# Kernel tuning notes

Measured on AMD Instinct MI355X. Metric: run time of the kernel, lower is better.

The kernel has to match this reference:

```python
import jax, jax.numpy as jnp
import numpy as np

B, N1, N2, C1, C2, MLP_OUT = 16, 4096, 1024, 128, 256, 256


def setup_inputs() -> dict:
    key = jax.random.key(0)
    k = jax.random.split(key, 8)
    xyz1 = jax.random.normal(k[0], (B, N1, 3), dtype=jnp.float32)
    feat1 = jax.random.normal(k[1], (B, N1, C1), dtype=jnp.float32)
    xyz2 = jax.random.normal(k[2], (B, N2, 3), dtype=jnp.float32)
    feat2 = jax.random.normal(k[3], (B, N2, C2), dtype=jnp.float32)
    d_in = C1 + C2
    W1 = jax.random.normal(k[4], (d_in, MLP_OUT), dtype=jnp.float32) / np.sqrt(d_in)
    b1 = jnp.zeros((MLP_OUT,), dtype=jnp.float32)
    W2 = jax.random.normal(k[5], (MLP_OUT, MLP_OUT), dtype=jnp.float32) / np.sqrt(MLP_OUT)
    b2 = jnp.zeros((MLP_OUT,), dtype=jnp.float32)
    return {"xyz1": xyz1, "feat1": feat1, "xyz2": xyz2, "feat2": feat2,
            "W1": W1, "b1": b1, "W2": W2, "b2": b2}


def reference(xyz1, feat1, xyz2, feat2, W1, b1, W2, b2):
    # squared pairwise distances [B, N1, N2]
    dists = jnp.sum((xyz1[:, :, None, :] - xyz2[:, None, :, :]) ** 2, axis=-1)
    # 3 nearest neighbors (smallest distances)
    neg_d3, idx = jax.lax.top_k(-dists, 3)      # [B, N1, 3]
    d3 = jnp.maximum(-neg_d3, 1e-10)
    w = 1.0 / d3
    w = w / jnp.sum(w, axis=-1, keepdims=True)   # [B, N1, 3]
    # gather neighbor features: [B, N1, 3, C2]
    neighbor_feats = jax.vmap(lambda f, i: f[i])(feat2, idx)
    interpolated = jnp.sum(w[..., None] * neighbor_feats, axis=2)  # [B, N1, C2]
    new_feat = jnp.concatenate([interpolated, feat1], axis=-1)     # [B, N1, C2+C1]
    h = jax.nn.relu(new_feat @ W1 + b1)
    return jax.nn.relu(h @ W2 + b2)
```

## Files before the change

### kernel.cpp

```cpp
#include <hip/hip_runtime.h>
#include <cstdint>
#include <cstddef>

typedef unsigned short ushort_t;
typedef unsigned int uint_t;

typedef __bf16 bf16x8 __attribute__((ext_vector_type(8)));
typedef float floatx4 __attribute__((ext_vector_type(4)));

#define B_ 16
#define N1_ 4096
#define N2_ 1024
#define C1_ 128
#define C2_ 256
#define DIN_ 384
#define DOUT_ 256
#define M_ (B_ * N1_)

#define ASTRIDE 392
#define HSTRIDE 264


__device__ __forceinline__ ushort_t f2bf(float f) {
  unsigned int u = __builtin_bit_cast(unsigned int, f);
  u = (u + 0x7fffu + ((u >> 16) & 1u)) >> 16;
  return (ushort_t)u;
}


__global__ __launch_bounds__(256) void prep_kernel(
    const float* __restrict__ W1, const float* __restrict__ W2,
    ushort_t* __restrict__ W1s, ushort_t* __restrict__ W2s) {
  int e = blockIdx.x * 256 + threadIdx.x;
  if (e < DOUT_ * DIN_) {
    int kk = e & 31, n = (e >> 5) & 255, t = e >> 13;
    W1s[e] = f2bf(W1[(size_t)(t * 32 + kk) * DOUT_ + n]);
  }
  if (e < DOUT_ * DOUT_) {
    int kk = e & 31, n = (e >> 5) & 255, t = e >> 13;
    W2s[e] = f2bf(W2[(size_t)(t * 32 + kk) * DOUT_ + n]);
  }
}


__device__ __forceinline__ void ins_exact(float& s0, float& s1, float& s2,
                                          int& i0, int& i1, int& i2,
                                          float d, int p) {
  float ns2 = __builtin_amdgcn_fmed3f(d, s1, s2);
  float ns1 = __builtin_amdgcn_fmed3f(d, s0, s1);
  float ns0 = fminf(d, s0);
  bool c0 = d < s0, c1 = d < s1, c2 = d < s2;
  i2 = c1 ? i1 : (c2 ? p : i2);
  i1 = c0 ? i0 : (c1 ? p : i1);
  i0 = c0 ? p : i0;
  s0 = ns0; s1 = ns1; s2 = ns2;
}

__device__ __forceinline__ void ins_merge(float& s0, float& s1, float& s2,
                                          int& i0, int& i1, int& i2,
                                          float e, int j) {
  bool t0 = (e < s0) || (e == s0 && j < i0);
  bool t1 = (e < s1) || (e == s1 && j < i1);
  bool t2 = (e < s2) || (e == s2 && j < i2);
  s2 = t1 ? s1 : (t2 ? e : s2);
  i2 = t1 ? i1 : (t2 ? j : i2);
  s1 = t0 ? s0 : (t1 ? e : s1);
  i1 = t0 ? i0 : (t1 ? j : i1);
  s0 = t0 ? e : s0;
  i0 = t0 ? j : i0;
}

__global__ __launch_bounds__(256) void knn_kernel(
    const float* __restrict__ xyz1, const float* __restrict__ xyz2,
    int* __restrict__ idx_out, float* __restrict__ w_out) {
  __shared__ float4 xs4[N2_];
  int b = blockIdx.x >> 7;
  int n1base = (blockIdx.x & 127) << 5;
  const float* p2 = xyz2 + (size_t)b * N2_ * 3;
  for (int i = threadIdx.x; i < N2_; i += 256) {
    const float* s = p2 + 3 * i;
    xs4[i] = make_float4(s[0], s[1], s[2], 0.0f);
  }
  __syncthreads();

  int g = threadIdx.x >> 3;
  int sub = threadIdx.x & 7;
  int row = b * N1_ + n1base + g;
  const float* p1 = xyz1 + (size_t)row * 3;
  float x1 = p1[0], y1 = p1[1], z1 = p1[2];

  float s0 = 3.0e38f, s1 = 3.0e38f, s2 = 3.0e38f;
  int i0 = 0, i1 = 0, i2 = 0;

  int p = sub;
#pragma unroll 8
  for (int t = 0; t < N2_ / 8; ++t) {
    float4 qv = xs4[p];
    float dx = x1 - qv.x;
    float dy = y1 - qv.y;
    float dz = z1 - qv.z;
    float d = dx * dx + dy * dy + dz * dz;
    ins_exact(s0, s1, s2, i0, i1, i2, d, p);
    p += 8;
  }

#pragma unroll
  for (int mm = 1; mm <= 4; mm <<= 1) {
    float e0 = __shfl_xor(s0, mm), e1 = __shfl_xor(s1, mm), e2 = __shfl_xor(s2, mm);
    int j0 = __shfl_xor(i0, mm), j1 = __shfl_xor(i1, mm), j2 = __shfl_xor(i2, mm);
    ins_merge(s0, s1, s2, i0, i1, i2, e0, j0);
    ins_merge(s0, s1, s2, i0, i1, i2, e1, j1);
    ins_merge(s0, s1, s2, i0, i1, i2, e2, j2);
  }

  if (sub == 0) {
    float r0 = 1.0f / fmaxf(s0, 1e-10f);
    float r1 = 1.0f / fmaxf(s1, 1e-10f);
    float r2 = 1.0f / fmaxf(s2, 1e-10f);
    float s = 1.0f / (r0 + r1 + r2);
    int base = row * 3;
    idx_out[base + 0] = i0;
    idx_out[base + 1] = i1;
    idx_out[base + 2] = i2;
    w_out[base + 0] = r0 * s;
    w_out[base + 1] = r1 * s;
    w_out[base + 2] = r2 * s;
  }
}


__global__ __launch_bounds__(256, 3) void fused_kernel(
    const float* __restrict__ feat1, const float* __restrict__ feat2,
    const int* __restrict__ idx, const float* __restrict__ w,
    const ushort_t* __restrict__ W1s, const float* __restrict__ b1,
    const ushort_t* __restrict__ W2s, const float* __restrict__ b2,
    float* __restrict__ out) {
  __shared__ ushort_t As[64 * ASTRIDE];
  const int tid = threadIdx.x;
  const int wave = tid >> 6;
  const int lane = tid & 63;
  const int m = lane & 15;
  const int q = lane >> 4;
  const int row0 = blockIdx.x * 64;
  const int b = row0 >> 12;

  const int b_off = (wave * 64 + m) * 32 + q * 8;

  bf16x8 bf0[4], bf1[4];
#pragma unroll
  for (int j = 0; j < 4; ++j) bf0[j] = *(const bf16x8*)(W1s + b_off + j * 512);

#pragma unroll 8
  for (int it = 0; it < 16; ++it) {
    int rl = wave * 16 + it;
    int row = row0 + rl;
    const int* ip = idx + (size_t)row * 3;
    const float* wp = w + (size_t)row * 3;
    int i0 = ip[0], i1 = ip[1], i2 = ip[2];
    float w0 = wp[0], w1 = wp[1], w2 = wp[2];

    const float4* f0 = (const float4*)(feat2 + ((size_t)b * N2_ + i0) * C2_);
    const float4* f1 = (const float4*)(feat2 + ((size_t)b * N2_ + i1) * C2_);
    const float4* f2 = (const float4*)(feat2 + ((size_t)b * N2_ + i2) * C2_);
    float4 a = f0[lane];
    float4 c = f1[lane];
    float4 d = f2[lane];
    float vx = w0 * a.x + w1 * c.x + w2 * d.x;
    float vy = w0 * a.y + w1 * c.y + w2 * d.y;
    float vz = w0 * a.z + w1 * c.z + w2 * d.z;
    float vw = w0 * a.w + w1 * c.w + w2 * d.w;
    uint_t lo = (uint_t)f2bf(vx) | ((uint_t)f2bf(vy) << 16);
    uint_t hi = (uint_t)f2bf(vz) | ((uint_t)f2bf(vw) << 16);
    *(uint2*)&As[rl * ASTRIDE + 4 * lane] = make_uint2(lo, hi);

    float2 t1 = ((const float2*)(feat1 + (size_t)row * C1_))[lane];
    uint_t pk = (uint_t)f2bf(t1.x) | ((uint_t)f2bf(t1.y) << 16);
    *(uint_t*)&As[rl * ASTRIDE + 256 + 2 * lane] = pk;
  }
  __syncthreads();

  floatx4 acc[4][4];
#pragma unroll
  for (int i = 0; i < 4; ++i)
#pragma unroll
    for (int j = 0; j < 4; ++j) acc[i][j] = (floatx4)0.0f;

  {
    bf16x8 af[4];
#pragma unroll
    for (int t = 0; t < 12; t += 2) {
#pragma unroll
      for (int j = 0; j < 4; ++j)
        bf1[j] = *(const bf16x8*)(W1s + (size_t)(t + 1) * 8192 + b_off + j * 512);
#pragma unroll
      for (int i = 0; i < 4; ++i)
        af[i] = *(const bf16x8*)&As[(m + 16 * i) * ASTRIDE + t * 32 + q * 8];
#pragma unroll
      for (int i = 0; i < 4; ++i)
#pragma unroll
        for (int j = 0; j < 4; ++j)
          acc[i][j] = __builtin_amdgcn_mfma_f32_16x16x32_bf16(af[i], bf0[j],
                                                              acc[i][j], 0, 0, 0);
      if (t + 2 < 12) {
#pragma unroll
        for (int j = 0; j < 4; ++j)
          bf0[j] = *(const bf16x8*)(W1s + (size_t)(t + 2) * 8192 + b_off + j * 512);
      }
#pragma unroll
      for (int i = 0; i < 4; ++i)
        af[i] = *(const bf16x8*)&As[(m + 16 * i) * ASTRIDE + (t + 1) * 32 + q * 8];
#pragma unroll
      for (int i = 0; i < 4; ++i)
#pragma unroll
        for (int j = 0; j < 4; ++j)
          acc[i][j] = __builtin_amdgcn_mfma_f32_16x16x32_bf16(af[i], bf1[j],
                                                              acc[i][j], 0, 0, 0);
    }
  }

#pragma unroll
  for (int j = 0; j < 4; ++j) bf0[j] = *(const bf16x8*)(W2s + b_off + j * 512);

  __syncthreads();

  ushort_t* HS = As;
#pragma unroll
  for (int j = 0; j < 4; ++j) {
    int col = wave * 64 + j * 16 + m;
    float bv = b1[col];
#pragma unroll
    for (int i = 0; i < 4; ++i)
#pragma unroll
      for (int r = 0; r < 4; ++r) {
        int row = i * 16 + q * 4 + r;
        float v = acc[i][j][r] + bv;
        v = v > 0.0f ? v : 0.0f;
        HS[row * HSTRIDE + col] = f2bf(v);
      }
  }
  __syncthreads();

  floatx4 acc2[4][4];
#pragma unroll
  for (int i = 0; i < 4; ++i)
#pragma unroll
    for (int j = 0; j < 4; ++j) acc2[i][j] = (floatx4)0.0f;

  {
    bf16x8 af[4];
#pragma unroll
    for (int t = 0; t < 8; t += 2) {
#pragma unroll
      for (int j = 0; j < 4; ++j)
        bf1[j] = *(const bf16x8*)(W2s + (size_t)(t + 1) * 8192 + b_off + j * 512);
#pragma unroll
      for (int i = 0; i < 4; ++i)
        af[i] = *(const bf16x8*)&HS[(m + 16 * i) * HSTRIDE + t * 32 + q * 8];
#pragma unroll
      for (int i = 0; i < 4; ++i)
#pragma unroll
        for (int j = 0; j < 4; ++j)
          acc2[i][j] = __builtin_amdgcn_mfma_f32_16x16x32_bf16(af[i], bf0[j],
                                                               acc2[i][j], 0, 0, 0);
      if (t + 2 < 8) {
#pragma unroll
        for (int j = 0; j < 4; ++j)
          bf0[j] = *(const bf16x8*)(W2s + (size_t)(t + 2) * 8192 + b_off + j * 512);
      }
#pragma unroll
      for (int i = 0; i < 4; ++i)
        af[i] = *(const bf16x8*)&HS[(m + 16 * i) * HSTRIDE + (t + 1) * 32 + q * 8];
#pragma unroll
      for (int i = 0; i < 4; ++i)
#pragma unroll
        for (int j = 0; j < 4; ++j)
          acc2[i][j] = __builtin_amdgcn_mfma_f32_16x16x32_bf16(af[i], bf1[j],
                                                               acc2[i][j], 0, 0, 0);
    }
  }

#pragma unroll
  for (int j = 0; j < 4; ++j) {
    int col = wave * 64 + j * 16 + m;
    float bv = b2[col];
#pragma unroll
    for (int i = 0; i < 4; ++i)
#pragma unroll
      for (int r = 0; r < 4; ++r) {
        int row = i * 16 + q * 4 + r;
        float v = acc2[i][j][r] + bv;
        v = v > 0.0f ? v : 0.0f;
        out[(size_t)(row0 + row) * DOUT_ + col] = v;
      }
  }
}


constexpr size_t OFF_W1S = 0;
constexpr size_t OFF_W2S = OFF_W1S + 196608;
constexpr size_t OFF_IDX = OFF_W2S + 131072;
constexpr size_t OFF_W = OFF_IDX + 786432;
constexpr size_t WS_TOTAL = OFF_W + 786432;

extern "C" void kernel_launch(void* const* d_in, const int* in_sizes, int n_in,
                              void* d_out, int out_size, void* d_ws, size_t ws_size,
                              hipStream_t stream) {
  const float* xyz1 = (const float*)d_in[0];
  const float* feat1 = (const float*)d_in[1];
  const float* xyz2 = (const float*)d_in[2];
  const float* feat2 = (const float*)d_in[3];
  const float* W1 = (const float*)d_in[4];
  const float* b1 = (const float*)d_in[5];
  const float* W2 = (const float*)d_in[6];
  const float* b2 = (const float*)d_in[7];

  if (ws_size < WS_TOTAL) return;

  char* ws = (char*)d_ws;
  ushort_t* W1s = (ushort_t*)(ws + OFF_W1S);
  ushort_t* W2s = (ushort_t*)(ws + OFF_W2S);
  int* idx = (int*)(ws + OFF_IDX);
  float* w = (float*)(ws + OFF_W);

  prep_kernel<<<384, 256, 0, stream>>>(W1, W2, W1s, W2s);
  knn_kernel<<<B_ * (N1_ / 32), 256, 0, stream>>>(xyz1, xyz2, idx, w);
  fused_kernel<<<M_ / 64, 256, 0, stream>>>(feat1, feat2, idx, w, W1s, b1, W2s,
                                            b2, (float*)d_out);
}
```

Measured before the change: 196.4 us.

## Use one thread per query in KNN and 8-wave 2x4 tiling in fused MLP

The KNN kernel drops the 8-lane split per query and its shuffle merge. Each thread now scans all 1024 reference points itself, in 128-thread blocks, and writes the result directly. The fused MLP kernel goes from 4 to 8 waves per 64-row block, with each wave computing a 32x64 output tile instead of 64x64. Register double-buffering of weight fragments is removed so that more waves can be resident. This trades explicit load pipelining and LDS fragment reuse for higher occupancy, and the KNN change cuts the grid to 512 blocks, which may leave the GPU underfilled.

New measurement: 233.4 us. +18.8%, slower.

```diff
diff --git a/kernel.cpp b/kernel.cpp
--- a/kernel.cpp
+++ b/kernel.cpp
@@ -43,93 +43,61 @@
 }
 
 
-__device__ __forceinline__ void ins_exact(float& s0, float& s1, float& s2,
-                                          int& i0, int& i1, int& i2,
-                                          float d, int p) {
-  float ns2 = __builtin_amdgcn_fmed3f(d, s1, s2);
-  float ns1 = __builtin_amdgcn_fmed3f(d, s0, s1);
-  float ns0 = fminf(d, s0);
-  bool c0 = d < s0, c1 = d < s1, c2 = d < s2;
-  i2 = c1 ? i1 : (c2 ? p : i2);
-  i1 = c0 ? i0 : (c1 ? p : i1);
-  i0 = c0 ? p : i0;
-  s0 = ns0; s1 = ns1; s2 = ns2;
-}
-
-__device__ __forceinline__ void ins_merge(float& s0, float& s1, float& s2,
-                                          int& i0, int& i1, int& i2,
-                                          float e, int j) {
-  bool t0 = (e < s0) || (e == s0 && j < i0);
-  bool t1 = (e < s1) || (e == s1 && j < i1);
-  bool t2 = (e < s2) || (e == s2 && j < i2);
-  s2 = t1 ? s1 : (t2 ? e : s2);
-  i2 = t1 ? i1 : (t2 ? j : i2);
-  s1 = t0 ? s0 : (t1 ? e : s1);
-  i1 = t0 ? i0 : (t1 ? j : i1);
-  s0 = t0 ? e : s0;
-  i0 = t0 ? j : i0;
-}
-
-__global__ __launch_bounds__(256) void knn_kernel(
+__global__ __launch_bounds__(128) void knn_kernel(
     const float* __restrict__ xyz1, const float* __restrict__ xyz2,
     int* __restrict__ idx_out, float* __restrict__ w_out) {
   __shared__ float4 xs4[N2_];
-  int b = blockIdx.x >> 7;
-  int n1base = (blockIdx.x & 127) << 5;
+  const int b = blockIdx.x >> 5;
+  const int chunk = blockIdx.x & 31;
   const float* p2 = xyz2 + (size_t)b * N2_ * 3;
-  for (int i = threadIdx.x; i < N2_; i += 256) {
+  for (int i = threadIdx.x; i < N2_; i += 128) {
     const float* s = p2 + 3 * i;
     xs4[i] = make_float4(s[0], s[1], s[2], 0.0f);
   }
   __syncthreads();
 
-  int g = threadIdx.x >> 3;
-  int sub = threadIdx.x & 7;
-  int row = b * N1_ + n1base + g;
+  const int row = b * N1_ + chunk * 128 + threadIdx.x;
   const float* p1 = xyz1 + (size_t)row * 3;
-  float x1 = p1[0], y1 = p1[1], z1 = p1[2];
+  const float x1 = p1[0], y1 = p1[1], z1 = p1[2];
 
   float s0 = 3.0e38f, s1 = 3.0e38f, s2 = 3.0e38f;
   int i0 = 0, i1 = 0, i2 = 0;
 
-  int p = sub;
-#pragma unroll 8
-  for (int t = 0; t < N2_ / 8; ++t) {
-    float4 qv = xs4[p];
-    float dx = x1 - qv.x;
-    float dy = y1 - qv.y;
-    float dz = z1 - qv.z;
-    float d = dx * dx + dy * dy + dz * dz;
-    ins_exact(s0, s1, s2, i0, i1, i2, d, p);
-    p += 8;
-  }
-
-#pragma unroll
-  for (int mm = 1; mm <= 4; mm <<= 1) {
-    float e0 = __shfl_xor(s0, mm), e1 = __shfl_xor(s1, mm), e2 = __shfl_xor(s2, mm);
-    int j0 = __shfl_xor(i0, mm), j1 = __shfl_xor(i1, mm), j2 = __shfl_xor(i2, mm);
-    ins_merge(s0, s1, s2, i0, i1, i2, e0, j0);
-    ins_merge(s0, s1, s2, i0, i1, i2, e1, j1);
-    ins_merge(s0, s1, s2, i0, i1, i2, e2, j2);
-  }
-
-  if (sub == 0) {
-    float r0 = 1.0f / fmaxf(s0, 1e-10f);
-    float r1 = 1.0f / fmaxf(s1, 1e-10f);
-    float r2 = 1.0f / fmaxf(s2, 1e-10f);
-    float s = 1.0f / (r0 + r1 + r2);
-    int base = row * 3;
-    idx_out[base + 0] = i0;
-    idx_out[base + 1] = i1;
-    idx_out[base + 2] = i2;
-    w_out[base + 0] = r0 * s;
-    w_out[base + 1] = r1 * s;
-    w_out[base + 2] = r2 * s;
-  }
-}
-
-
-__global__ __launch_bounds__(256, 3) void fused_kernel(
+  for (int o = 0; o < N2_; o += 16) {
+#pragma unroll
+    for (int i = 0; i < 16; ++i) {
+      float4 qv = xs4[o + i];
+      float dx = x1 - qv.x;
+      float dy = y1 - qv.y;
+      float dz = z1 - qv.z;
+      float d = dx * dx + dy * dy + dz * dz;
+      bool c0 = d < s0, c1 = d < s1, c2 = d < s2;
+      float ns2 = __builtin_amdgcn_fmed3f(d, s1, s2);
+      float ns1 = __builtin_amdgcn_fmed3f(d, s0, s1);
+      float ns0 = fminf(d, s0);
+      int p = o + i;
+      i2 = c1 ? i1 : (c2 ? p : i2);
+      i1 = c0 ? i0 : (c1 ? p : i1);
+      i0 = c0 ? p : i0;
+      s0 = ns0; s1 = ns1; s2 = ns2;
+    }
+  }
+
+  float r0 = 1.0f / fmaxf(s0, 1e-10f);
+  float r1 = 1.0f / fmaxf(s1, 1e-10f);
+  float r2 = 1.0f / fmaxf(s2, 1e-10f);
+  float s = 1.0f / (r0 + r1 + r2);
+  int base = row * 3;
+  idx_out[base + 0] = i0;
+  idx_out[base + 1] = i1;
+  idx_out[base + 2] = i2;
+  w_out[base + 0] = r0 * s;
+  w_out[base + 1] = r1 * s;
+  w_out[base + 2] = r2 * s;
+}
+
+
+__global__ __launch_bounds__(512, 6) void fused_kernel(
     const float* __restrict__ feat1, const float* __restrict__ feat2,
     const int* __restrict__ idx, const float* __restrict__ w,
     const ushort_t* __restrict__ W1s, const float* __restrict__ b1,
@@ -141,18 +109,16 @@
   const int lane = tid & 63;
   const int m = lane & 15;
   const int q = lane >> 4;
+  const int wm = wave & 1;
+  const int wn = wave >> 1;
   const int row0 = blockIdx.x * 64;
   const int b = row0 >> 12;
 
-  const int b_off = (wave * 64 + m) * 32 + q * 8;
-
-  bf16x8 bf0[4], bf1[4];
-#pragma unroll
-  for (int j = 0; j < 4; ++j) bf0[j] = *(const bf16x8*)(W1s + b_off + j * 512);
-
-#pragma unroll 8
-  for (int it = 0; it < 16; ++it) {
-    int rl = wave * 16 + it;
+  const int b_off = (wn * 64 + m) * 32 + q * 8;
+
+#pragma unroll
+  for (int it = 0; it < 8; ++it) {
+    int rl = wave * 8 + it;
     int row = row0 + rl;
     const int* ip = idx + (size_t)row * 3;
     const float* wp = w + (size_t)row * 3;
@@ -179,60 +145,40 @@
   }
   __syncthreads();
 
-  floatx4 acc[4][4];
-#pragma unroll
-  for (int i = 0; i < 4; ++i)
+  floatx4 acc[2][4];
+#pragma unroll
+  for (int i = 0; i < 2; ++i)
 #pragma unroll
     for (int j = 0; j < 4; ++j) acc[i][j] = (floatx4)0.0f;
 
-  {
-    bf16x8 af[4];
-#pragma unroll
-    for (int t = 0; t < 12; t += 2) {
+#pragma unroll 2
+  for (int t = 0; t < 12; ++t) {
+    bf16x8 bfr[4], af[2];
+#pragma unroll
+    for (int j = 0; j < 4; ++j)
+      bfr[j] = *(const bf16x8*)(W1s + (size_t)t * 8192 + b_off + j * 512);
+#pragma unroll
+    for (int i = 0; i < 2; ++i)
+      af[i] = *(const bf16x8*)&As[(wm * 32 + m + 16 * i) * ASTRIDE + t * 32 + q * 8];
+#pragma unroll
+    for (int i = 0; i < 2; ++i)
 #pragma unroll
       for (int j = 0; j < 4; ++j)
-        bf1[j] = *(const bf16x8*)(W1s + (size_t)(t + 1) * 8192 + b_off + j * 512);
-#pragma unroll
-      for (int i = 0; i < 4; ++i)
-        af[i] = *(const bf16x8*)&As[(m + 16 * i) * ASTRIDE + t * 32 + q * 8];
-#pragma unroll
-      for (int i = 0; i < 4; ++i)
-#pragma unroll
-        for (int j = 0; j < 4; ++j)
-          acc[i][j] = __builtin_amdgcn_mfma_f32_16x16x32_bf16(af[i], bf0[j],
-                                                              acc[i][j], 0, 0, 0);
-      if (t + 2 < 12) {
-#pragma unroll
-        for (int j = 0; j < 4; ++j)
-          bf0[j] = *(const bf16x8*)(W1s + (size_t)(t + 2) * 8192 + b_off + j * 512);
-      }
-#pragma unroll
-      for (int i = 0; i < 4; ++i)
-        af[i] = *(const bf16x8*)&As[(m + 16 * i) * ASTRIDE + (t + 1) * 32 + q * 8];
-#pragma unroll
-      for (int i = 0; i < 4; ++i)
-#pragma unroll
-        for (int j = 0; j < 4; ++j)
-          acc[i][j] = __builtin_amdgcn_mfma_f32_16x16x32_bf16(af[i], bf1[j],
-                                                              acc[i][j], 0, 0, 0);
-    }
-  }
-
-#pragma unroll
-  for (int j = 0; j < 4; ++j) bf0[j] = *(const bf16x8*)(W2s + b_off + j * 512);
-
+        acc[i][j] = __builtin_amdgcn_mfma_f32_16x16x32_bf16(af[i], bfr[j],
+                                                            acc[i][j], 0, 0, 0);
+  }
   __syncthreads();
 
   ushort_t* HS = As;
 #pragma unroll
   for (int j = 0; j < 4; ++j) {
-    int col = wave * 64 + j * 16 + m;
+    int col = wn * 64 + j * 16 + m;
     float bv = b1[col];
 #pragma unroll
-    for (int i = 0; i < 4; ++i)
+    for (int i = 0; i < 2; ++i)
 #pragma unroll
       for (int r = 0; r < 4; ++r) {
-        int row = i * 16 + q * 4 + r;
+        int row = wm * 32 + i * 16 + q * 4 + r;
         float v = acc[i][j][r] + bv;
         v = v > 0.0f ? v : 0.0f;
         HS[row * HSTRIDE + col] = f2bf(v);
@@ -240,54 +186,38 @@
   }
   __syncthreads();
 
-  floatx4 acc2[4][4];
-#pragma unroll
-  for (int i = 0; i < 4; ++i)
+  floatx4 acc2[2][4];
+#pragma unroll
+  for (int i = 0; i < 2; ++i)
 #pragma unroll
     for (int j = 0; j < 4; ++j) acc2[i][j] = (floatx4)0.0f;
 
-  {
-    bf16x8 af[4];
-#pragma unroll
-    for (int t = 0; t < 8; t += 2) {
+#pragma unroll 2
+  for (int t = 0; t < 8; ++t) {
+    bf16x8 bfr[4], af[2];
+#pragma unroll
+    for (int j = 0; j < 4; ++j)
+      bfr[j] = *(const bf16x8*)(W2s + (size_t)t * 8192 + b_off + j * 512);
+#pragma unroll
+    for (int i = 0; i < 2; ++i)
+      af[i] = *(const bf16x8*)&HS[(wm * 32 + m + 16 * i) * HSTRIDE + t * 32 + q * 8];
+#pragma unroll
+    for (int i = 0; i < 2; ++i)
 #pragma unroll
       for (int j = 0; j < 4; ++j)
-        bf1[j] = *(const bf16x8*)(W2s + (size_t)(t + 1) * 8192 + b_off + j * 512);
-#pragma unroll
-      for (int i = 0; i < 4; ++i)
-        af[i] = *(const bf16x8*)&HS[(m + 16 * i) * HSTRIDE + t * 32 + q * 8];
-#pragma unroll
-      for (int i = 0; i < 4; ++i)
-#pragma unroll
-        for (int j = 0; j < 4; ++j)
-          acc2[i][j] = __builtin_amdgcn_mfma_f32_16x16x32_bf16(af[i], bf0[j],
-                                                               acc2[i][j], 0, 0, 0);
-      if (t + 2 < 8) {
-#pragma unroll
-        for (int j = 0; j < 4; ++j)
-          bf0[j] = *(const bf16x8*)(W2s + (size_t)(t + 2) * 8192 + b_off + j * 512);
-      }
-#pragma unroll
-      for (int i = 0; i < 4; ++i)
-        af[i] = *(const bf16x8*)&HS[(m + 16 * i) * HSTRIDE + (t + 1) * 32 + q * 8];
-#pragma unroll
-      for (int i = 0; i < 4; ++i)
-#pragma unroll
-        for (int j = 0; j < 4; ++j)
-          acc2[i][j] = __builtin_amdgcn_mfma_f32_16x16x32_bf16(af[i], bf1[j],
-                                                               acc2[i][j], 0, 0, 0);
-    }
+        acc2[i][j] = __builtin_amdgcn_mfma_f32_16x16x32_bf16(af[i], bfr[j],
+                                                             acc2[i][j], 0, 0, 0);
   }
 
 #pragma unroll
   for (int j = 0; j < 4; ++j) {
-    int col = wave * 64 + j * 16 + m;
+    int col = wn * 64 + j * 16 + m;
     float bv = b2[col];
 #pragma unroll
-    for (int i = 0; i < 4; ++i)
+    for (int i = 0; i < 2; ++i)
 #pragma unroll
       for (int r = 0; r < 4; ++r) {
-        int row = i * 16 + q * 4 + r;
+        int row = wm * 32 + i * 16 + q * 4 + r;
         float v = acc2[i][j][r] + bv;
         v = v > 0.0f ? v : 0.0f;
         out[(size_t)(row0 + row) * DOUT_ + col] = v;
@@ -323,7 +253,7 @@
   float* w = (float*)(ws + OFF_W);
 
   prep_kernel<<<384, 256, 0, stream>>>(W1, W2, W1s, W2s);
-  knn_kernel<<<B_ * (N1_ / 32), 256, 0, stream>>>(xyz1, xyz2, idx, w);
-  fused_kernel<<<M_ / 64, 256, 0, stream>>>(feat1, feat2, idx, w, W1s, b1, W2s,
+  knn_kernel<<<B_ * (N1_ / 128), 128, 0, stream>>>(xyz1, xyz2, idx, w);
+  fused_kernel<<<M_ / 64, 512, 0, stream>>>(feat1, feat2, idx, w, W1s, b1, W2s,
                                             b2, (float*)d_out);
 }
```
